# Kernel tuning notes

Measured on AMD Instinct MI355X. Metric: run time of the kernel, lower is better.

The kernel has to match this reference:

```python
import jax, jax.numpy as jnp
import numpy as np

B, T, E, H, ENC, V = 32, 128, 256, 512, 512, 10000


def setup_inputs() -> dict:
    key = jax.random.key(0)
    ks = jax.random.split(key, 16)
    s = 0.02
    return {
        "text_vectors": jax.random.normal(ks[0], (B, ENC), dtype=jnp.float32),
        "texts": jax.random.randint(ks[1], (B, T), 0, V),
        "lengths": jax.random.randint(ks[2], (B,), 1, T + 1),
        "start_idx": 1,
        "emb_table": jax.random.normal(ks[3], (V, E), dtype=jnp.float32) * s,
        "W_ih": jax.random.normal(ks[4], (4 * H, E + H + ENC), dtype=jnp.float32) * s,
        "b_ih": jnp.zeros((4 * H,), dtype=jnp.float32),
        "W_hh": jax.random.normal(ks[5], (4 * H, H), dtype=jnp.float32) * s,
        "b_hh": jnp.zeros((4 * H,), dtype=jnp.float32),
        "Wo_w": jax.random.normal(ks[6], (H, ENC), dtype=jnp.float32) * s,
        "Wo_b": jnp.zeros((H,), dtype=jnp.float32),
        "Wh_w": jax.random.normal(ks[7], (H, ENC), dtype=jnp.float32) * s,
        "Wh_b": jnp.zeros((H,), dtype=jnp.float32),
        "Wc_w": jax.random.normal(ks[8], (H, ENC), dtype=jnp.float32) * s,
        "Wc_b": jnp.zeros((H,), dtype=jnp.float32),
        "Wv_w": jax.random.normal(ks[9], (V, H), dtype=jnp.float32) * s,
        "Wv_b": jnp.zeros((V,), dtype=jnp.float32),
    }


def reference(text_vectors, texts, lengths, start_idx, emb_table,
              W_ih, b_ih, W_hh, b_hh, Wo_w, Wo_b, Wh_w, Wh_b, Wc_w, Wc_b,
              Wv_w, Wv_b):
    del lengths  # unused in the original forward loop
    batch = texts.shape[0]
    # initial previous-token embedding = embedding of start token, broadcast
    y0 = jnp.broadcast_to(emb_table[start_idx], (batch, emb_table.shape[1]))
    o = text_vectors @ Wo_w.T + Wo_b          # [B, H], constant across steps
    h0 = text_vectors @ Wh_w.T + Wh_b          # [B, H]
    c0 = text_vectors @ Wc_w.T + Wc_b          # [B, H]
    embedded_texts = emb_table[texts.T]        # [T, B, E]

    def step(carry, emb_t):
        h, c, y = carry
        x = jnp.concatenate((y, o, text_vectors), axis=1)  # [B, E+H+ENC]
        gates = x @ W_ih.T + b_ih + h @ W_hh.T + b_hh      # [B, 4H]
        i_g, f_g, g_g, o_g = jnp.split(gates, 4, axis=1)
        c = jax.nn.sigmoid(f_g) * c + jax.nn.sigmoid(i_g) * jnp.tanh(g_g)
        h = jax.nn.sigmoid(o_g) * jnp.tanh(c)
        return (h, c, emb_t), h

    _, hs = jax.lax.scan(step, (h0, c0, y0), embedded_texts)  # hs: [T, B, H]
    logits = jnp.einsum('tbh,vh->btv', hs, Wv_w) + Wv_b        # [B, T, V]
    return logits
```

## Files before the change

kernel.cpp:

```cpp
#include <hip/hip_runtime.h>
#include <math.h>

#define Bx   32
#define Tx   128
#define Ex   256
#define Hx   512
#define ENCx 512
#define Vx   10000
#define G4   2048

#define RBLK 64
#define UPB  8
#define KREC 768
#define KPAD 776

typedef __bf16 bf16x8 __attribute__((ext_vector_type(8)));
typedef float  f32x4  __attribute__((ext_vector_type(4)));

#define MFMA16 __builtin_amdgcn_mfma_f32_16x16x32_bf16

__device__ __forceinline__ float sigm(float x) { return 1.0f / (1.0f + expf(-x)); }

__device__ __forceinline__ void store_u32_wt(uint32_t* p, uint32_t v) {
  asm volatile("global_store_dword %0, %1, off sc0 sc1" :: "v"(p), "v"(v) : "memory");
}
__device__ __forceinline__ void store_b16_wt(__bf16* p, uint32_t v) {
  asm volatile("global_store_short %0, %1, off sc0 sc1" :: "v"(p), "v"(v) : "memory");
}

__global__ __launch_bounds__(256) void k_init(
    const float* __restrict__ tv,
    const float* __restrict__ Wo_w, const float* __restrict__ Wo_b,
    const float* __restrict__ Wh_w, const float* __restrict__ Wh_b,
    const float* __restrict__ Wc_w, const float* __restrict__ Wc_b,
    float* __restrict__ o, __bf16* __restrict__ hinit, float* __restrict__ c0) {
  int tid = blockIdx.x * blockDim.x + threadIdx.x;
  int which = tid / (Bx * Hx);
  int r = tid - which * (Bx * Hx);
  int b = r >> 9, j = r & (Hx - 1);
  const float* W; const float* bias;
  if (which == 0)      { W = Wo_w; bias = Wo_b; }
  else if (which == 1) { W = Wh_w; bias = Wh_b; }
  else                 { W = Wc_w; bias = Wc_b; }
  const float* x = tv + b * ENCx;
  const float* w = W + (size_t)j * ENCx;
  float acc = bias[j];
#pragma unroll 8
  for (int k = 0; k < ENCx; k++) acc += x[k] * w[k];
  if (which == 0)      o[b * Hx + j] = acc;
  else if (which == 1) hinit[b * Hx + j] = (__bf16)acc;
  else                 c0[j * Bx + b] = acc;
}

__global__ __launch_bounds__(256) void k_const(
    const float* __restrict__ tv, const float* __restrict__ o,
    const float* __restrict__ W_ih, const float* __restrict__ b_ih,
    const float* __restrict__ b_hh, float* __restrict__ constC,
    int* __restrict__ flags) {
  int tid = blockIdx.x * blockDim.x + threadIdx.x;
  if (tid < RBLK) flags[tid] = 0;
  int b = tid >> 11, g = tid & (G4 - 1);
  const float* w = W_ih + (size_t)g * (Ex + Hx + ENCx);
  float acc = b_ih[g] + b_hh[g];
  const float* ob = o + b * Hx;
#pragma unroll 8
  for (int k = 0; k < Hx; k++) acc += ob[k] * w[Ex + k];
  const float* xb = tv + b * ENCx;
#pragma unroll 8
  for (int k = 0; k < ENCx; k++) acc += xb[k] * w[Ex + Hx + k];
  constC[b * G4 + g] = acc;
}

__global__ __launch_bounds__(256) void k_cvt(
    const float* __restrict__ src, __bf16* __restrict__ dst, int n) {
  int i = (blockIdx.x * blockDim.x + threadIdx.x) * 4;
  if (i < n) {
    float4 v = *(const float4*)(src + i);
    dst[i + 0] = (__bf16)v.x; dst[i + 1] = (__bf16)v.y;
    dst[i + 2] = (__bf16)v.z; dst[i + 3] = (__bf16)v.w;
  }
}

__global__ __launch_bounds__(256) void k_cvt2d(
    const float* __restrict__ src, __bf16* __restrict__ dst) {
  int idx = (blockIdx.x * 256 + threadIdx.x) * 4;
  int row = idx >> 8, col = idx & 255;
  float4 v = *(const float4*)(src + (size_t)row * 1280 + col);
  dst[idx + 0] = (__bf16)v.x; dst[idx + 1] = (__bf16)v.y;
  dst[idx + 2] = (__bf16)v.z; dst[idx + 3] = (__bf16)v.w;
}

__global__ __launch_bounds__(256) void k_rec(
    const __bf16* __restrict__ Whb,
    const __bf16* __restrict__ Wihb,
    const __bf16* __restrict__ embb,
    const int* __restrict__ texts, const int* __restrict__ sidx,
    const float* __restrict__ constC,
    const float* __restrict__ c0,
    const __bf16* __restrict__ hinit,
    __bf16* __restrict__ hs2,
    int* __restrict__ flags) {
  __shared__ __bf16 Ws[2 * 16][KPAD];
  __shared__ __bf16 Hs[32][KPAD];
  __shared__ float  Cs[32][33];
  __shared__ int    tokL[Bx * Tx];

  const int q = threadIdx.x;
  const int nb = blockIdx.x;
  const int u0 = nb * UPB;
  const int lane = q & 63, wave = q >> 6;
  const int mt = wave & 1, jt = wave >> 1;
  const int fm = lane & 15, fk = (lane >> 4) * 8;
  const int cr = (lane >> 4) * 4, cc = lane & 15;
  const int s0tok = sidx[0];

  {
    const int row = q >> 3;
    const int wr = (row & 3) * Hx + u0 + (row >> 2);
    const __bf16* wh = Whb + (size_t)wr * Hx;
    const __bf16* wy = Wihb + (size_t)wr * Ex;
#pragma unroll
    for (int r = 0; r < 12; r++) {
      const int col = ((q & 7) + 8 * r) * 8;
      bf16x8 v = (col < Hx) ? *(const bf16x8*)(wh + col)
                            : *(const bf16x8*)(wy + col - Hx);
      *(bf16x8*)&Ws[row][col] = v;
    }
  }
#pragma unroll
  for (int r = 0; r < 16; r++) tokL[q + 256 * r] = texts[q + 256 * r];
#pragma unroll
  for (int r = 0; r < 8; r++) {
    const int hv = q + 256 * r;
    const int row = hv >> 6, col = (hv & 63) * 8;
    *(bf16x8*)&Hs[row][col] = *(const bf16x8*)(hinit + row * Hx + col);
  }
#pragma unroll
  for (int r = 0; r < 4; r++) {
    const int vy = q + 256 * r;
    const int row = vy >> 5, col = (vy & 31) * 8;
    *(bf16x8*)&Hs[row][Hx + col] = *(const bf16x8*)(embb + (size_t)s0tok * Ex + col);
  }

  const int eb = q >> 3, eu = q & 7, eu4 = (q & 7) * 4;
  float creg = c0[(u0 + eu) * Bx + eb];
  const float cc0v = constC[eb * G4 + 0 * Hx + u0 + eu];
  const float cc1v = constC[eb * G4 + 1 * Hx + u0 + eu];
  const float cc2v = constC[eb * G4 + 2 * Hx + u0 + eu];
  const float cc3v = constC[eb * G4 + 3 * Hx + u0 + eu];

  __syncthreads();

  for (int t = 0; t < Tx; t++) {
    f32x4 accA = {0.f, 0.f, 0.f, 0.f}, accB = {0.f, 0.f, 0.f, 0.f};
    const __bf16* ha = &Hs[mt * 16 + fm][0];
    const __bf16* wrow = &Ws[jt * 16 + fm][0];
#pragma unroll
    for (int ks = 0; ks < 24; ks += 2) {
      accA = MFMA16(*(const bf16x8*)(ha + ks * 32 + fk),
                    *(const bf16x8*)(wrow + ks * 32 + fk), accA, 0, 0, 0);
      accB = MFMA16(*(const bf16x8*)(ha + ks * 32 + 32 + fk),
                    *(const bf16x8*)(wrow + ks * 32 + 32 + fk), accB, 0, 0, 0);
    }
    {
      const f32x4 acc = accA + accB;
#pragma unroll
      for (int r = 0; r < 4; r++) Cs[mt * 16 + cr + r][jt * 16 + cc] = acc[r];
    }
    __syncthreads();

    bf16x8 yv[4];
    const int tn = t + 1;
    if (tn < Tx) {
#pragma unroll
      for (int r = 0; r < 4; r++) {
        const int vy = q + 256 * r;
        const int row = vy >> 5, col = (vy & 31) * 8;
        const int tok = tokL[row * Tx + tn - 1];
        yv[r] = *(const bf16x8*)(embb + (size_t)tok * Ex + col);
      }
    }
    {
      const float pi = Cs[eb][eu4 + 0] + cc0v;
      const float pf = Cs[eb][eu4 + 1] + cc1v;
      const float pg = Cs[eb][eu4 + 2] + cc2v;
      const float po = Cs[eb][eu4 + 3] + cc3v;
      const float cn = sigm(pf) * creg + sigm(pi) * tanhf(pg);
      creg = cn;
      const __bf16 hb = (__bf16)(sigm(po) * tanhf(cn));
      const uint32_t hu = (uint32_t)__builtin_bit_cast(unsigned short, hb);
      store_b16_wt(hs2 + (size_t)t * (Bx * Hx) + eb * Hx + u0 + eu, hu);
    }
    if (tn < Tx) {
#pragma unroll
      for (int r = 0; r < 4; r++) {
        const int vy = q + 256 * r;
        const int row = vy >> 5, col = (vy & 31) * 8;
        *(bf16x8*)&Hs[row][Hx + col] = yv[r];
      }
    }
    asm volatile("s_waitcnt vmcnt(0)" ::: "memory");
    __syncthreads();

    if (t < Tx - 1) {
      if (q == 0) store_u32_wt((uint32_t*)&flags[nb], t + 1);
      const __bf16* src = hs2 + (size_t)t * (Bx * Hx);
      const int sbase = wave * 16;
      const int myfl = (nb >= sbase && nb < sbase + 16) ? (nb - sbase) : -1;
      const int prow = lane >> 1, phalf = lane & 1;
      bf16x8 pv0, pv1, pv2, pv3, pv4, pv5, pv6, pv7;
      uint32_t done = 0, prevm = 0;
      for (;;) {
        uint32_t fv = 0;
        const bool last = ((done | prevm) == 0xFFu);
        if (!last && lane < 16) {
          if (lane == myfl) {
            fv = 0x7FFFFFFFu;
          } else {
            const uint32_t* fp = (const uint32_t*)&flags[sbase + lane];
            asm volatile("global_load_dword %0, %1, off sc0 sc1"
                         : "=v"(fv) : "v"(fp));
          }
        }
        asm volatile("s_waitcnt vmcnt(0)" ::: "memory");
        __builtin_amdgcn_sched_barrier(0);
#define WR_P(P) if (prevm & (1u << P)) \
  *(bf16x8*)&Hs[prow][(sbase + 2 * P) * 8 + phalf * 8] = pv##P;
        WR_P(0) WR_P(1) WR_P(2) WR_P(3) WR_P(4) WR_P(5) WR_P(6) WR_P(7)
#undef WR_P
        done |= prevm;
        if (done == 0xFFu) break;
        const bool rdy = (lane < 16) && ((int)fv >= t + 1);
        const unsigned long long bl = __ballot(rdy);
        const uint32_t r16 = (uint32_t)bl & 0xFFFFu;
        const uint32_t x = r16 & (r16 >> 1);
        const uint32_t pairm = (x & 1u) | ((x >> 1) & 2u) | ((x >> 2) & 4u)
                             | ((x >> 3) & 8u) | ((x >> 4) & 16u)
                             | ((x >> 5) & 32u) | ((x >> 6) & 64u)
                             | ((x >> 7) & 128u);
        const uint32_t newm = pairm & ~done;
        prevm = newm;
#define LD_P(P) if (newm & (1u << P)) { \
  const __bf16* p_ = src + prow * Hx + (sbase + 2 * P) * 8 + phalf * 8; \
  asm volatile("global_load_dwordx4 %0, %1, off sc0 sc1" : "=v"(pv##P) : "v"(p_)); }
        LD_P(0) LD_P(1) LD_P(2) LD_P(3) LD_P(4) LD_P(5) LD_P(6) LD_P(7)
#undef LD_P
      }
    }
    __syncthreads();
  }
}

#define PM 128
#define PN 128
#define PK 32
#define PKP 40

__global__ __launch_bounds__(256) void k_proj_mfma(
    const __bf16* __restrict__ A,
    const __bf16* __restrict__ Bw,
    const float* __restrict__ bias, float* __restrict__ C) {
  __shared__ __bf16 As[PM][PKP];
  __shared__ __bf16 Bs[PN][PKP];
  const int m0 = blockIdx.x * PM;
  const int n0 = blockIdx.y * PN;
  const int t = threadIdx.x;
  const int wave = t >> 6, lane = t & 63;
  const int wm = (wave & 1) * 64, wn = (wave >> 1) * 64;
  const int fm = lane & 15, fk = (lane >> 4) * 8;
  const int sr = t >> 2, sk = (t & 3) * 8;

  const int n1 = min(n0 + sr, Vx - 1);
  const int n2 = min(n0 + sr + 64, Vx - 1);
  const int g1 = m0 + sr, g2 = m0 + sr + 64;
  const int r1 = ((g1 & 127) << 5) | (g1 >> 7);
  const int r2 = ((g2 & 127) << 5) | (g2 >> 7);

  f32x4 acc[4][4];
#pragma unroll
  for (int i = 0; i < 4; i++)
#pragma unroll
    for (int j = 0; j < 4; j++) acc[i][j] = (f32x4){0.f, 0.f, 0.f, 0.f};

  for (int k0 = 0; k0 < Hx; k0 += PK) {
    __syncthreads();
    *(bf16x8*)&As[sr][sk]      = *(const bf16x8*)&A[(size_t)r1 * Hx + k0 + sk];
    *(bf16x8*)&As[sr + 64][sk] = *(const bf16x8*)&A[(size_t)r2 * Hx + k0 + sk];
    *(bf16x8*)&Bs[sr][sk]      = *(const bf16x8*)&Bw[(size_t)n1 * Hx + k0 + sk];
    *(bf16x8*)&Bs[sr + 64][sk] = *(const bf16x8*)&Bw[(size_t)n2 * Hx + k0 + sk];
    __syncthreads();
    bf16x8 af[4], bfr[4];
#pragma unroll
    for (int i = 0; i < 4; i++) af[i]  = *(const bf16x8*)&As[wm + i * 16 + fm][fk];
#pragma unroll
    for (int j = 0; j < 4; j++) bfr[j] = *(const bf16x8*)&Bs[wn + j * 16 + fm][fk];
#pragma unroll
    for (int i = 0; i < 4; i++)
#pragma unroll
      for (int j = 0; j < 4; j++)
        acc[i][j] = MFMA16(af[i], bfr[j], acc[i][j], 0, 0, 0);
  }

  const int cr = (lane >> 4) * 4, cc = lane & 15;
#pragma unroll
  for (int i = 0; i < 4; i++) {
#pragma unroll
    for (int r = 0; r < 4; r++) {
      const int m = m0 + wm + i * 16 + cr + r;
      float* crow = C + (size_t)m * Vx;
#pragma unroll
      for (int j = 0; j < 4; j++) {
        const int n = n0 + wn + j * 16 + cc;
        if (n < Vx) crow[n] = acc[i][j][r] + bias[n];
      }
    }
  }
}

extern "C" void kernel_launch(void* const* d_in, const int* in_sizes, int n_in,
                              void* d_out, int out_size, void* d_ws, size_t ws_size,
                              hipStream_t stream) {
  const float* tv     = (const float*)d_in[0];
  const int*   texts  = (const int*)d_in[1];
  const int*   sidx   = (const int*)d_in[3];
  const float* emb    = (const float*)d_in[4];
  const float* W_ih   = (const float*)d_in[5];
  const float* b_ih   = (const float*)d_in[6];
  const float* W_hh   = (const float*)d_in[7];
  const float* b_hh   = (const float*)d_in[8];
  const float* Wo_w   = (const float*)d_in[9];
  const float* Wo_b   = (const float*)d_in[10];
  const float* Wh_w   = (const float*)d_in[11];
  const float* Wh_b   = (const float*)d_in[12];
  const float* Wc_w   = (const float*)d_in[13];
  const float* Wc_b   = (const float*)d_in[14];
  const float* Wv_w   = (const float*)d_in[15];
  const float* Wv_b   = (const float*)d_in[16];
  float* out = (float*)d_out;

  float* ws     = (float*)d_ws;
  float* o      = ws;
  float* c0     = o + Bx * Hx;
  float* constC = c0 + Hx * Bx;
  int*   flags  = (int*)(constC + (size_t)Bx * G4);
  __bf16* bfb   = (__bf16*)(ws + 98816);
  __bf16* hinit = bfb;
  __bf16* hs2   = hinit + Bx * Hx;
  __bf16* Wvb   = hs2 + (size_t)Bx * Tx * Hx;
  __bf16* Whb   = Wvb + (size_t)Vx * Hx;
  __bf16* embb  = Whb + (size_t)G4 * Hx;
  __bf16* Wihb  = embb + (size_t)Vx * Ex;

  hipLaunchKernelGGL(k_cvt, dim3((Vx * Hx / 4 + 255) / 256), dim3(256), 0, stream,
                     Wv_w, Wvb, Vx * Hx);
  hipLaunchKernelGGL(k_cvt, dim3((G4 * Hx / 4 + 255) / 256), dim3(256), 0, stream,
                     W_hh, Whb, G4 * Hx);
  hipLaunchKernelGGL(k_cvt, dim3((Vx * Ex / 4 + 255) / 256), dim3(256), 0, stream,
                     emb, embb, Vx * Ex);
  hipLaunchKernelGGL(k_cvt2d, dim3(G4 * Ex / 4 / 256), dim3(256), 0, stream,
                     W_ih, Wihb);
  hipLaunchKernelGGL(k_init, dim3(192), dim3(256), 0, stream,
                     tv, Wo_w, Wo_b, Wh_w, Wh_b, Wc_w, Wc_b, o, hinit, c0);
  hipLaunchKernelGGL(k_const, dim3(256), dim3(256), 0, stream,
                     tv, o, W_ih, b_ih, b_hh, constC, flags);
  hipLaunchKernelGGL(k_rec, dim3(RBLK), dim3(256), 0, stream,
                     Whb, Wihb, embb, texts, sidx, constC, c0, hinit, hs2, flags);
  hipLaunchKernelGGL(k_proj_mfma, dim3((Bx * Tx) / PM, (Vx + PN - 1) / PN), dim3(256), 0, stream,
                     hs2, Wvb, Wv_b, out);
}
```

Baseline: 975.4 us.

## Replace per-block flags with step-tagged hidden-state words for inter-block sync

The per-block flag plus separate data-load handshake in the persistent recurrent kernel is replaced by 32-bit words that each pack the bf16 hidden value with the step number. Consumers poll the data itself and retry only the chunks whose tag does not match, using a double-buffered exchange array indexed by step parity. This removes one round trip of flag polling before the data fetch on each step's global barrier. In exchange each poll moves twice as many bytes and every thread polls the whole hidden state, and the embedding prefetch is no longer overlapped with the gate math.

Result: faster. 865.7 us (-11.2%).

```diff
diff --git a/kernel.cpp b/kernel.cpp
--- a/kernel.cpp
+++ b/kernel.cpp
@@ -16,6 +16,7 @@
 
 typedef __bf16 bf16x8 __attribute__((ext_vector_type(8)));
 typedef float  f32x4  __attribute__((ext_vector_type(4)));
+typedef uint32_t u32x4 __attribute__((ext_vector_type(4)));
 
 #define MFMA16 __builtin_amdgcn_mfma_f32_16x16x32_bf16
 
@@ -23,9 +24,6 @@
 
 __device__ __forceinline__ void store_u32_wt(uint32_t* p, uint32_t v) {
   asm volatile("global_store_dword %0, %1, off sc0 sc1" :: "v"(p), "v"(v) : "memory");
-}
-__device__ __forceinline__ void store_b16_wt(__bf16* p, uint32_t v) {
-  asm volatile("global_store_short %0, %1, off sc0 sc1" :: "v"(p), "v"(v) : "memory");
 }
 
 __global__ __launch_bounds__(256) void k_init(
@@ -56,9 +54,9 @@
     const float* __restrict__ tv, const float* __restrict__ o,
     const float* __restrict__ W_ih, const float* __restrict__ b_ih,
     const float* __restrict__ b_hh, float* __restrict__ constC,
-    int* __restrict__ flags) {
+    uint32_t* __restrict__ tgd) {
   int tid = blockIdx.x * blockDim.x + threadIdx.x;
-  if (tid < RBLK) flags[tid] = 0;
+  if (tid < 2 * Bx * Hx) tgd[tid] = 0;
   int b = tid >> 11, g = tid & (G4 - 1);
   const float* w = W_ih + (size_t)g * (Ex + Hx + ENCx);
   float acc = b_ih[g] + b_hh[g];
@@ -99,7 +97,7 @@
     const float* __restrict__ c0,
     const __bf16* __restrict__ hinit,
     __bf16* __restrict__ hs2,
-    int* __restrict__ flags) {
+    uint32_t* __restrict__ tgd) {
   __shared__ __bf16 Ws[2 * 16][KPAD];
   __shared__ __bf16 Hs[32][KPAD];
   __shared__ float  Cs[32][33];
@@ -169,17 +167,6 @@
     }
     __syncthreads();
 
-    bf16x8 yv[4];
-    const int tn = t + 1;
-    if (tn < Tx) {
-#pragma unroll
-      for (int r = 0; r < 4; r++) {
-        const int vy = q + 256 * r;
-        const int row = vy >> 5, col = (vy & 31) * 8;
-        const int tok = tokL[row * Tx + tn - 1];
-        yv[r] = *(const bf16x8*)(embb + (size_t)tok * Ex + col);
-      }
-    }
     {
       const float pi = Cs[eb][eu4 + 0] + cc0v;
       const float pf = Cs[eb][eu4 + 1] + cc1v;
@@ -189,62 +176,50 @@
       creg = cn;
       const __bf16 hb = (__bf16)(sigm(po) * tanhf(cn));
       const uint32_t hu = (uint32_t)__builtin_bit_cast(unsigned short, hb);
-      store_b16_wt(hs2 + (size_t)t * (Bx * Hx) + eb * Hx + u0 + eu, hu);
-    }
-    if (tn < Tx) {
+      store_u32_wt(tgd + (size_t)(t & 1) * (Bx * Hx) + eb * Hx + u0 + eu,
+                   ((uint32_t)(t + 1) << 16) | hu);
+      hs2[(size_t)t * (Bx * Hx) + eb * Hx + u0 + eu] = hb;
+    }
+    if (t + 1 < Tx) {
 #pragma unroll
       for (int r = 0; r < 4; r++) {
         const int vy = q + 256 * r;
         const int row = vy >> 5, col = (vy & 31) * 8;
-        *(bf16x8*)&Hs[row][Hx + col] = yv[r];
+        const int tok = tokL[row * Tx + t];
+        *(bf16x8*)&Hs[row][Hx + col] = *(const bf16x8*)(embb + (size_t)tok * Ex + col);
       }
-    }
-    asm volatile("s_waitcnt vmcnt(0)" ::: "memory");
-    __syncthreads();
-
-    if (t < Tx - 1) {
-      if (q == 0) store_u32_wt((uint32_t*)&flags[nb], t + 1);
-      const __bf16* src = hs2 + (size_t)t * (Bx * Hx);
-      const int sbase = wave * 16;
-      const int myfl = (nb >= sbase && nb < sbase + 16) ? (nb - sbase) : -1;
-      const int prow = lane >> 1, phalf = lane & 1;
-      bf16x8 pv0, pv1, pv2, pv3, pv4, pv5, pv6, pv7;
-      uint32_t done = 0, prevm = 0;
+      const uint32_t* src = tgd + (size_t)(t & 1) * (Bx * Hx);
+      const uint32_t want = (uint32_t)(t + 1);
+      u32x4 vv[16];
+      uint32_t miss = 0xFFFFu;
       for (;;) {
-        uint32_t fv = 0;
-        const bool last = ((done | prevm) == 0xFFu);
-        if (!last && lane < 16) {
-          if (lane == myfl) {
-            fv = 0x7FFFFFFFu;
-          } else {
-            const uint32_t* fp = (const uint32_t*)&flags[sbase + lane];
-            asm volatile("global_load_dword %0, %1, off sc0 sc1"
-                         : "=v"(fv) : "v"(fp));
-          }
+#pragma unroll
+        for (int i = 0; i < 16; i++) if (miss & (1u << i)) {
+          const int c = i * 64 + lane;
+          const uint32_t* p_ = src + (c >> 5) * Hx + wave * 128 + (c & 31) * 4;
+          asm volatile("global_load_dwordx4 %0, %1, off sc0 sc1"
+                       : "=v"(vv[i]) : "v"(p_));
         }
         asm volatile("s_waitcnt vmcnt(0)" ::: "memory");
         __builtin_amdgcn_sched_barrier(0);
-#define WR_P(P) if (prevm & (1u << P)) \
-  *(bf16x8*)&Hs[prow][(sbase + 2 * P) * 8 + phalf * 8] = pv##P;
-        WR_P(0) WR_P(1) WR_P(2) WR_P(3) WR_P(4) WR_P(5) WR_P(6) WR_P(7)
-#undef WR_P
-        done |= prevm;
-        if (done == 0xFFu) break;
-        const bool rdy = (lane < 16) && ((int)fv >= t + 1);
-        const unsigned long long bl = __ballot(rdy);
-        const uint32_t r16 = (uint32_t)bl & 0xFFFFu;
-        const uint32_t x = r16 & (r16 >> 1);
-        const uint32_t pairm = (x & 1u) | ((x >> 1) & 2u) | ((x >> 2) & 4u)
-                             | ((x >> 3) & 8u) | ((x >> 4) & 16u)
-                             | ((x >> 5) & 32u) | ((x >> 6) & 64u)
-                             | ((x >> 7) & 128u);
-        const uint32_t newm = pairm & ~done;
-        prevm = newm;
-#define LD_P(P) if (newm & (1u << P)) { \
-  const __bf16* p_ = src + prow * Hx + (sbase + 2 * P) * 8 + phalf * 8; \
-  asm volatile("global_load_dwordx4 %0, %1, off sc0 sc1" : "=v"(pv##P) : "v"(p_)); }
-        LD_P(0) LD_P(1) LD_P(2) LD_P(3) LD_P(4) LD_P(5) LD_P(6) LD_P(7)
-#undef LD_P
+        uint32_t nmiss = 0;
+#pragma unroll
+        for (int i = 0; i < 16; i++) if (miss & (1u << i)) {
+          const bool ok = (vv[i].x >> 16) == want && (vv[i].y >> 16) == want &&
+                          (vv[i].z >> 16) == want && (vv[i].w >> 16) == want;
+          if (!ok) nmiss |= (1u << i);
+        }
+        miss = nmiss;
+        if (__ballot(miss != 0) == 0) break;
+      }
+#pragma unroll
+      for (int i = 0; i < 16; i++) {
+        const int c = i * 64 + lane;
+        const int row = c >> 5, col = wave * 128 + (c & 31) * 4;
+        uint2 d;
+        d.x = (vv[i].x & 0xFFFFu) | (vv[i].y << 16);
+        d.y = (vv[i].z & 0xFFFFu) | (vv[i].w << 16);
+        *(uint2*)&Hs[row][col] = d;
       }
     }
     __syncthreads();
@@ -342,8 +317,8 @@
   float* o      = ws;
   float* c0     = o + Bx * Hx;
   float* constC = c0 + Hx * Bx;
-  int*   flags  = (int*)(constC + (size_t)Bx * G4);
-  __bf16* bfb   = (__bf16*)(ws + 98816);
+  uint32_t* tgd = (uint32_t*)(constC + (size_t)Bx * G4);
+  __bf16* bfb   = (__bf16*)(ws + 98304 + 2 * Bx * Hx);
   __bf16* hinit = bfb;
   __bf16* hs2   = hinit + Bx * Hx;
   __bf16* Wvb   = hs2 + (size_t)Bx * Tx * Hx;
@@ -362,9 +337,9 @@
   hipLaunchKernelGGL(k_init, dim3(192), dim3(256), 0, stream,
                      tv, Wo_w, Wo_b, Wh_w, Wh_b, Wc_w, Wc_b, o, hinit, c0);
   hipLaunchKernelGGL(k_const, dim3(256), dim3(256), 0, stream,
-                     tv, o, W_ih, b_ih, b_hh, constC, flags);
+                     tv, o, W_ih, b_ih, b_hh, constC, tgd);
   hipLaunchKernelGGL(k_rec, dim3(RBLK), dim3(256), 0, stream,
-                     Whb, Wihb, embb, texts, sidx, constC, c0, hinit, hs2, flags);
+                     Whb, Wihb, embb, texts, sidx, constC, c0, hinit, hs2, tgd);
   hipLaunchKernelGGL(k_proj_mfma, dim3((Bx * Tx) / PM, (Vx + PN - 1) / PN), dim3(256), 0, stream,
                      hs2, Wvb, Wv_b, out);
 }
```
